# Kernel tuning notes

Measured on AMD Instinct MI355X. Metric: run time of the kernel, lower is better.

## Reference

```python
import math
import jax, jax.numpy as jnp
import numpy as np

B, S, D, H = 2, 2048, 2048, 16
HD = D // H
EPS = 1e-6


def _precompute_freqs_cis(dim, end, theta=500000.0):
    inv_freqs = 1.0 / theta ** (np.arange(0, dim, 2, dtype=np.float32) / dim)
    t = np.arange(end, dtype=np.float32)
    freqs = np.outer(t, inv_freqs).astype(np.float32)
    # [1, end, 1, dim//2, 2] matching torch stack(cos, sin, dim=4)
    return jnp.asarray(np.stack([np.cos(freqs)[None, :, None, :], np.sin(freqs)[None, :, None, :]], axis=4))


def setup_inputs() -> dict:
    key = jax.random.key(0)
    k1, k2, k3 = jax.random.split(key, 3)
    x = jax.random.normal(k1, (B, S, D), dtype=jnp.float32)
    w_qkv = jax.random.normal(k2, (3 * D, D), dtype=jnp.float32) * 0.02
    w_out = jax.random.normal(k3, (D, D), dtype=jnp.float32) * 0.02
    attn_scale = jnp.asarray(math.log2(S * S - S), dtype=jnp.float32)
    freqs_cis = _precompute_freqs_cis(HD, S)
    return {"x": x, "w_qkv": w_qkv, "w_out": w_out, "attn_scale": attn_scale, "freqs_cis": freqs_cis}


def _apply_rotary(q, k, fc):
    # q, k: [b, s, h, hd]; fc: [1, s, 1, hd//2, 2]
    b, s, h, hd = q.shape
    qk = jnp.concatenate([q, k], axis=2).reshape(b, s, 2 * h, hd // 2, 2)
    real = qk[..., 0] * fc[..., 0] - qk[..., 1] * fc[..., 1]
    imag = qk[..., 1] * fc[..., 0] + qk[..., 0] * fc[..., 1]
    rot = jnp.stack([real, imag], axis=-1).reshape(b, s, 2 * h, hd)
    return rot[:, :, :h], rot[:, :, h:]


def reference(x, w_qkv, w_out, attn_scale, freqs_cis):
    b, s, d = x.shape
    qkv = x @ w_qkv.T                      # [b, s, 3d]
    q, k, v = jnp.split(qkv, 3, axis=2)
    q = q.reshape(b, s, H, HD)
    k = k.reshape(b, s, H, HD)
    v = v.reshape(b, s, H, HD)
    q, k = _apply_rotary(q, k, freqs_cis[:, :s])
    # -> [b, h, s, hd]
    q = q.transpose(0, 2, 1, 3)
    k = k.transpose(0, 2, 1, 3)
    v = v.transpose(0, 2, 1, 3)
    # per-head L2 norm of q/k, learned scale on q
    q = q / (jnp.linalg.norm(q, axis=-1, keepdims=True) + EPS)
    k = k / (jnp.linalg.norm(k, axis=-1, keepdims=True) + EPS)
    q = q * attn_scale
    # causal SDPA with scale=1.0
    scores = jnp.einsum('bhqd,bhkd->bhqk', q, k)
    causal = jnp.tril(jnp.ones((s, s), dtype=bool))
    scores = jnp.where(causal, scores, -jnp.inf)
    attn = jax.nn.softmax(scores, axis=-1)
    out = jnp.einsum('bhqk,bhkd->bhqd', attn, v)
    out = out.transpose(0, 2, 1, 3).reshape(b, s, d)
    return out @ w_out.T
```

## Files before the change

kernel.cpp:

```cpp
#include <hip/hip_runtime.h>
#include <stdint.h>

#define B_  2
#define S_  2048
#define D_  2048
#define H_  16
#define HD_ 128
#define D3_ 6144

typedef unsigned short u16;
typedef __attribute__((ext_vector_type(8))) __bf16 bf16x8;
typedef __attribute__((ext_vector_type(4))) float f32x4;
typedef __attribute__((ext_vector_type(8))) u16  u16x8;
typedef __attribute__((ext_vector_type(2))) u16  u16x2;

__device__ inline u16 f2bf(float f) {
  union { float f; uint32_t u; } v; v.f = f;
  uint32_t r = v.u + 0x7FFFu + ((v.u >> 16) & 1u);
  return (u16)(r >> 16);
}
__device__ inline float bf2f(u16 u) {
  union { float f; uint32_t u; } v; v.u = ((uint32_t)u) << 16;
  return v.f;
}
__device__ inline void gload_lds16(const void* g, void* l) {
  __builtin_amdgcn_global_load_lds((const __attribute__((address_space(1))) uint32_t*)g,
                                   (__attribute__((address_space(3))) uint32_t*)l, 16, 0, 0);
}

#define TILE_SYNC() do { \
    asm volatile("s_waitcnt lgkmcnt(0)" ::: "memory"); \
    asm volatile("s_waitcnt vmcnt(0)" ::: "memory"); \
    __builtin_amdgcn_s_barrier(); \
    asm volatile("" ::: "memory"); \
  } while (0)

__global__ __launch_bounds__(256) void castk(const float* __restrict__ in, u16* __restrict__ out, int n) {
  int i = blockIdx.x * 256 + threadIdx.x;
  int n8 = n >> 3;
  if (i < n8) {
    f32x4 a = ((const f32x4*)in)[2*i];
    f32x4 b = ((const f32x4*)in)[2*i + 1];
    u16x8 o;
#pragma unroll
    for (int j = 0; j < 4; ++j) o[j] = f2bf(a[j]);
#pragma unroll
    for (int j = 0; j < 4; ++j) o[4+j] = f2bf(b[j]);
    ((u16x8*)out)[i] = o;
  }
}

template<int BF16OUT>
__global__ __launch_bounds__(512, 2) void gemm8(const u16* __restrict__ A, const u16* __restrict__ Bw,
                                                void* __restrict__ Cp, int M, int N, int K) {
  __shared__ __align__(16) u16 lds_[65536];
  char* ldsb = (char*)lds_;
  const int tid = threadIdx.x;
  const int w = tid >> 6, l = tid & 63;
  const int lr = l & 15, lg = l >> 4;
  const int wr = w >> 2, wc = w & 3;
  const int nbn = (int)gridDim.x;
  const int nwg = nbn * (int)gridDim.y;
  const int bid = (int)(blockIdx.y * gridDim.x + blockIdx.x);
  const int swz = (bid & 7) * (nwg >> 3) + (bid >> 3);
  const int bm = swz / nbn, bn = swz % nbn;

  f32x4 acc[8][4] = {};

  int row4[4], col4[4];
#pragma unroll
  for (int i = 0; i < 4; ++i) {
    int off = i*8192 + tid*16;
    row4[i] = off >> 7;
    col4[i] = (off & 127) ^ ((row4[i] & 7) << 4);
  }
  const size_t rs = (size_t)K * 2;
  const char* Ab = (const char*)A + (size_t)bm * 256 * rs;
  const char* Bb = (const char*)Bw + (size_t)bn * 256 * rs;
  const int wb = w * 1024;

#define STG(T_) do { \
    char* dA_ = ldsb + ((T_)&1)*32768; \
    char* dB_ = ldsb + 65536 + ((T_)&1)*32768; \
    _Pragma("unroll") \
    for (int i_ = 0; i_ < 4; ++i_) \
      gload_lds16(Ab + (size_t)row4[i_]*rs + (size_t)(T_)*128 + col4[i_], dA_ + i_*8192 + wb); \
    _Pragma("unroll") \
    for (int i_ = 0; i_ < 4; ++i_) \
      gload_lds16(Bb + (size_t)row4[i_]*rs + (size_t)(T_)*128 + col4[i_], dB_ + i_*8192 + wb); \
  } while (0)

#define RD_A(dst, mf, ks) do { int row_ = wr*128 + (mf)*16 + lr; \
    dst = *(const bf16x8*)(La + row_*128 + (((ks)*64 + lg*16) ^ ((row_ & 7) << 4))); } while (0)
#define RD_B(dst, nf, ks) do { int row_ = wc*64 + (nf)*16 + lr; \
    dst = *(const bf16x8*)(Lb + row_*128 + (((ks)*64 + lg*16) ^ ((row_ & 7) << 4))); } while (0)

  const int NT = K >> 6;
  STG(0);
  TILE_SYNC();

  for (int T = 0; T < NT; ++T) {
    const char* La = ldsb + (T & 1)*32768;
    const char* Lb = ldsb + 65536 + (T & 1)*32768;
    if (T + 1 < NT) STG(T + 1);

    bf16x8 a0[4], a1[4], b0[4], b1[4];
#pragma unroll
    for (int mf = 0; mf < 4; ++mf) { RD_A(a0[mf], mf, 0); RD_A(a1[mf], mf, 1); }
#pragma unroll
    for (int nf = 0; nf < 4; ++nf) { RD_B(b0[nf], nf, 0); RD_B(b1[nf], nf, 1); }
#pragma unroll
    for (int mf = 0; mf < 4; ++mf)
#pragma unroll
      for (int nf = 0; nf < 4; ++nf) {
        acc[mf][nf] = __builtin_amdgcn_mfma_f32_16x16x32_bf16(a0[mf], b0[nf], acc[mf][nf], 0, 0, 0);
        acc[mf][nf] = __builtin_amdgcn_mfma_f32_16x16x32_bf16(a1[mf], b1[nf], acc[mf][nf], 0, 0, 0);
      }
#pragma unroll
    for (int mf = 0; mf < 4; ++mf) { RD_A(a0[mf], mf + 4, 0); RD_A(a1[mf], mf + 4, 1); }
#pragma unroll
    for (int mf = 0; mf < 4; ++mf)
#pragma unroll
      for (int nf = 0; nf < 4; ++nf) {
        acc[mf+4][nf] = __builtin_amdgcn_mfma_f32_16x16x32_bf16(a0[mf], b0[nf], acc[mf+4][nf], 0, 0, 0);
        acc[mf+4][nf] = __builtin_amdgcn_mfma_f32_16x16x32_bf16(a1[mf], b1[nf], acc[mf+4][nf], 0, 0, 0);
      }
    TILE_SYNC();
  }
#undef STG
#undef RD_A
#undef RD_B

#pragma unroll
  for (int mf = 0; mf < 8; ++mf)
#pragma unroll
    for (int nf = 0; nf < 4; ++nf)
#pragma unroll
      for (int j = 0; j < 4; ++j) {
        int m = bm*256 + wr*128 + mf*16 + lg*4 + j;
        int n = bn*256 + wc*64 + nf*16 + lr;
        float v = acc[mf][nf][j];
        if (BF16OUT) ((u16*)Cp)[(size_t)m * N + n] = f2bf(v);
        else         ((float*)Cp)[(size_t)m * N + n] = v;
      }
}

template<int BF16OUT>
__global__ __launch_bounds__(256, 2) void gemm_bt(const u16* __restrict__ A, const u16* __restrict__ Bw,
                                                  void* __restrict__ Cp, int M, int N, int K) {
  __shared__ __align__(16) u16 lds_[32768];
  char* ldsb = (char*)lds_;
  const int tid = threadIdx.x;
  const int w = tid >> 6, l = tid & 63;
  const int lr = l & 15, lg = l >> 4;
  const int nwg = (int)(gridDim.x * gridDim.y);
  const int bid = (int)(blockIdx.y * gridDim.x + blockIdx.x);
  const int swz = (bid & 7) * (nwg >> 3) + (bid >> 3);
  const int bm = swz / (int)gridDim.x, bn = swz % (int)gridDim.x;
  const int wr = w >> 1, wc = w & 1;

  f32x4 acc[4][4] = {};

  int row4[4], col4[4];
#pragma unroll
  for (int i = 0; i < 4; ++i) {
    int off = i*4096 + tid*16;
    row4[i] = off >> 7;
    col4[i] = (off & 127) ^ ((row4[i] & 7) << 4);
  }
  const size_t rs = (size_t)K * 2;
  const char* Ab = (const char*)A + (size_t)bm * 128 * rs;
  const char* Bb = (const char*)Bw + (size_t)bn * 128 * rs;
  const int wb = w * 1024;

#define STG(T_) do { \
    char* dA_ = ldsb + ((T_)&1)*16384; \
    char* dB_ = ldsb + 32768 + ((T_)&1)*16384; \
    _Pragma("unroll") \
    for (int i_ = 0; i_ < 4; ++i_) \
      gload_lds16(Ab + (size_t)row4[i_]*rs + (size_t)(T_)*128 + col4[i_], dA_ + i_*4096 + wb); \
    _Pragma("unroll") \
    for (int i_ = 0; i_ < 4; ++i_) \
      gload_lds16(Bb + (size_t)row4[i_]*rs + (size_t)(T_)*128 + col4[i_], dB_ + i_*4096 + wb); \
  } while (0)

  const int NT = K >> 6;
  STG(0);
  TILE_SYNC();

  for (int T = 0; T < NT; ++T) {
    const char* La = ldsb + (T & 1)*16384;
    const char* Lb = ldsb + 32768 + (T & 1)*16384;
    if (T + 1 < NT) STG(T + 1);

    bf16x8 af[4][2], bf[4][2];
#pragma unroll
    for (int mt = 0; mt < 4; ++mt) {
      int row = wr*64 + mt*16 + lr;
#pragma unroll
      for (int ks = 0; ks < 2; ++ks)
        af[mt][ks] = *(const bf16x8*)(La + row*128 + ((ks*64 + lg*16) ^ ((row & 7) << 4)));
    }
#pragma unroll
    for (int nt = 0; nt < 4; ++nt) {
      int row = wc*64 + nt*16 + lr;
#pragma unroll
      for (int ks = 0; ks < 2; ++ks)
        bf[nt][ks] = *(const bf16x8*)(Lb + row*128 + ((ks*64 + lg*16) ^ ((row & 7) << 4)));
    }
#pragma unroll
    for (int mt = 0; mt < 4; ++mt)
#pragma unroll
      for (int nt = 0; nt < 4; ++nt)
#pragma unroll
        for (int ks = 0; ks < 2; ++ks)
          acc[mt][nt] = __builtin_amdgcn_mfma_f32_16x16x32_bf16(af[mt][ks], bf[nt][ks], acc[mt][nt], 0, 0, 0);
    TILE_SYNC();
  }
#undef STG

#pragma unroll
  for (int mt = 0; mt < 4; ++mt)
#pragma unroll
    for (int nt = 0; nt < 4; ++nt)
#pragma unroll
      for (int j = 0; j < 4; ++j) {
        int m = bm*128 + wr*64 + mt*16 + lg*4 + j;
        int n = bn*128 + wc*64 + nt*16 + lr;
        float v = acc[mt][nt][j];
        if (BF16OUT) ((u16*)Cp)[(size_t)m * N + n] = f2bf(v);
        else         ((float*)Cp)[(size_t)m * N + n] = v;
      }
}

__global__ __launch_bounds__(256) void rope_norm(const u16* __restrict__ qkv, const float* __restrict__ fc,
                                                 const float* __restrict__ scale_p,
                                                 u16* __restrict__ Qo, u16* __restrict__ Ko) {
  int gid = blockIdx.x;
  int bs = gid >> 2;
  int s = bs & (S_ - 1);
  int b = bs >> 11;
  int w = threadIdx.x >> 6, l = threadIdx.x & 63;
  int h = (gid & 3)*4 + w;
  float2 cs = ((const float2*)fc)[(size_t)s*64 + l];
  float scale = scale_p[0] * 1.4426950408889634f;
  const u16* base = qkv + (size_t)bs * D3_;
  size_t obase = ((size_t)(b*H_ + h) * S_ + s) * HD_ + 2*l;
  {
    const u16* p = base + h*HD_ + 2*l;
    float x0 = bf2f(p[0]), x1 = bf2f(p[1]);
    float r0 = x0*cs.x - x1*cs.y;
    float r1 = x1*cs.x + x0*cs.y;
    float t = r0*r0 + r1*r1;
#pragma unroll
    for (int mk = 1; mk < 64; mk <<= 1) t += __shfl_xor(t, mk, 64);
    float inv = scale / (sqrtf(t) + 1e-6f);
    u16x2 o; o[0] = f2bf(r0*inv); o[1] = f2bf(r1*inv);
    *(u16x2*)(Qo + obase) = o;
  }
  {
    const u16* p = base + D_ + h*HD_ + 2*l;
    float x0 = bf2f(p[0]), x1 = bf2f(p[1]);
    float r0 = x0*cs.x - x1*cs.y;
    float r1 = x1*cs.x + x0*cs.y;
    float t = r0*r0 + r1*r1;
#pragma unroll
    for (int mk = 1; mk < 64; mk <<= 1) t += __shfl_xor(t, mk, 64);
    float inv = 1.0f / (sqrtf(t) + 1e-6f);
    u16x2 o; o[0] = f2bf(r0*inv); o[1] = f2bf(r1*inv);
    *(u16x2*)(Ko + obase) = o;
  }
}

__global__ __launch_bounds__(256) void v_trans(const u16* __restrict__ qkv, u16* __restrict__ Vt) {
  __shared__ u16 vt[64][136];
  int blk = blockIdx.x;
  int bh = blk >> 5, st = blk & 31;
  int b = bh >> 4, h = bh & 15;
  int s0 = st * 64;
  int tid = threadIdx.x;
#pragma unroll
  for (int i = 0; i < 4; ++i) {
    int idx = tid + i*256;
    int row = idx >> 4, ch = idx & 15;
    u16x8 v = *(const u16x8*)(qkv + (size_t)(b*S_ + s0 + row) * D3_ + 2*D_ + h*HD_ + ch*8);
    *(u16x8*)(&vt[row][ch*8]) = v;
  }
  __syncthreads();
#pragma unroll
  for (int p = 0; p < 2; ++p) {
    int d = p*64 + (tid >> 2);
    int q = (tid & 3) * 16;
    u16x8 t0, t1;
#pragma unroll
    for (int i = 0; i < 8; ++i) t0[i] = vt[q + i][d];
#pragma unroll
    for (int i = 0; i < 8; ++i) t1[i] = vt[q + 8 + i][d];
    u16* dst = Vt + ((size_t)bh * HD_ + d) * S_ + s0 + q;
    *(u16x8*)dst = t0;
    *(u16x8*)(dst + 8) = t1;
  }
}

__global__ __launch_bounds__(512) void flash_attn(const u16* __restrict__ Qh, const u16* __restrict__ Kh,
                                                  const u16* __restrict__ Vt, u16* __restrict__ AO) {
  __shared__ __align__(16) u16 lK[2][64*128];
  __shared__ __align__(16) u16 lV[128*64];
  __shared__ __align__(16) u16 lP[8][16*72];
  const int i0 = (int)blockIdx.x;
  const int k5 = i0 & 255;
  const int bh = k5 >> 3;
  const int jj = k5 & 7;
  const int qt = (i0 < 256) ? (15 - jj) : jj;
  const int tid = threadIdx.x, w = tid >> 6, l = tid & 63;
  const int lr = l & 15, lg = l >> 4;
  const int b = bh >> 4, h = bh & 15;

  bf16x8 qf[4];
  {
    const u16* qp = Qh + ((size_t)bh * S_ + qt*128 + w*16 + lr) * HD_ + lg*8;
#pragma unroll
    for (int ks = 0; ks < 4; ++ks) qf[ks] = *(const bf16x8*)(qp + ks*32);
  }
  float m[4], ls[4];
  f32x4 oacc[8] = {};
#pragma unroll
  for (int j = 0; j < 4; ++j) { m[j] = -__builtin_inff(); ls[j] = 0.f; }

  int krow[2], kcol[2], vrow[2], vcol[2], dstb[2];
#pragma unroll
  for (int p = 0; p < 2; ++p) {
    int off = p*8192 + tid*16;
    krow[p] = off >> 8; kcol[p] = (off & 255) ^ ((krow[p] & 7) << 4);
    vrow[p] = off >> 7; vcol[p] = (off & 127) ^ ((vrow[p] & 7) << 4);
    dstb[p] = p*8192 + w*1024;
  }
  const char* Kb = (const char*)(Kh + (size_t)bh * S_ * HD_);
  const char* Vb = (const char*)(Vt + (size_t)bh * HD_ * S_);

#define STAGE_K(nb, kt_) do {                                                       \
    _Pragma("unroll")                                                               \
    for (int p_ = 0; p_ < 2; ++p_)                                                  \
      gload_lds16(Kb + (size_t)((kt_)*64 + krow[p_])*256 + kcol[p_],                \
                  (char*)lK[nb] + dstb[p_]);                                        \
  } while (0)
#define STAGE_V(kt_) do {                                                           \
    _Pragma("unroll")                                                               \
    for (int p_ = 0; p_ < 2; ++p_)                                                  \
      gload_lds16(Vb + (size_t)vrow[p_]*(S_*2) + (kt_)*128 + vcol[p_],              \
                  (char*)lV + dstb[p_]);                                            \
  } while (0)

  const int nt = 2*qt + 2;
  STAGE_K(0, 0);
  STAGE_V(0);
  int cur = 0;
  for (int kt = 0; kt < nt; ++kt) {
    asm volatile("s_waitcnt vmcnt(2)" ::: "memory");
    __builtin_amdgcn_s_barrier();
    asm volatile("" ::: "memory");
    const char* lKb = (const char*)lK[cur];

    f32x4 sc[4] = {};
    __builtin_amdgcn_s_setprio(1);
#pragma unroll
    for (int f = 0; f < 4; ++f) {
      int row = f*16 + lr;
#pragma unroll
      for (int ks = 0; ks < 4; ++ks) {
        bf16x8 kf = *(const bf16x8*)(lKb + row*256 + ((ks*64 + lg*16) ^ ((row & 7) << 4)));
        sc[f] = __builtin_amdgcn_mfma_f32_16x16x32_bf16(qf[ks], kf, sc[f], 0, 0, 0);
      }
    }
    __builtin_amdgcn_s_setprio(0);
    if (kt < nt-1) STAGE_K(cur ^ 1, kt + 1);

    if (kt >= nt-2) {
#pragma unroll
      for (int f = 0; f < 4; ++f)
#pragma unroll
        for (int j = 0; j < 4; ++j)
          if (kt*64 + f*16 + lr > qt*128 + w*16 + lg*4 + j) sc[f][j] = -__builtin_inff();
    }
    float rm[4], resc[4], rowp[4];
#pragma unroll
    for (int j = 0; j < 4; ++j) {
      rm[j] = fmaxf(fmaxf(sc[0][j], sc[1][j]), fmaxf(sc[2][j], sc[3][j]));
      rm[j] = fmaxf(rm[j], __shfl_xor(rm[j], 1, 64));
      rm[j] = fmaxf(rm[j], __shfl_xor(rm[j], 2, 64));
      rm[j] = fmaxf(rm[j], __shfl_xor(rm[j], 4, 64));
      rm[j] = fmaxf(rm[j], __shfl_xor(rm[j], 8, 64));
      float mn = fmaxf(m[j], rm[j]);
      resc[j] = exp2f(m[j] - mn);
      m[j] = mn;
      rowp[j] = 0.f;
    }
#pragma unroll
    for (int f = 0; f < 4; ++f)
#pragma unroll
      for (int j = 0; j < 4; ++j) {
        float p = exp2f(sc[f][j] - m[j]);
        sc[f][j] = p;
        rowp[j] += p;
      }
#pragma unroll
    for (int j = 0; j < 4; ++j) {
      rowp[j] += __shfl_xor(rowp[j], 1, 64);
      rowp[j] += __shfl_xor(rowp[j], 2, 64);
      rowp[j] += __shfl_xor(rowp[j], 4, 64);
      rowp[j] += __shfl_xor(rowp[j], 8, 64);
      ls[j] = ls[j] * resc[j] + rowp[j];
    }
#pragma unroll
    for (int fd = 0; fd < 8; ++fd)
#pragma unroll
      for (int j = 0; j < 4; ++j) oacc[fd][j] *= resc[j];
#pragma unroll
    for (int f = 0; f < 4; ++f)
#pragma unroll
      for (int j = 0; j < 4; ++j)
        lP[w][(lg*4 + j)*72 + f*16 + lr] = f2bf(sc[f][j]);

    if (kt < nt-1) { asm volatile("s_waitcnt vmcnt(2)" ::: "memory"); }
    else           { asm volatile("s_waitcnt vmcnt(0)" ::: "memory"); }
    __builtin_amdgcn_s_barrier();
    asm volatile("" ::: "memory");
    __builtin_amdgcn_s_setprio(1);
#pragma unroll
    for (int ks = 0; ks < 2; ++ks) {
      bf16x8 pf = *(const bf16x8*)((const char*)lP[w] + lr*144 + ks*64 + lg*16);
#pragma unroll
      for (int fd = 0; fd < 8; ++fd) {
        int row = fd*16 + lr;
        bf16x8 vf = *(const bf16x8*)((const char*)lV + row*128 + ((ks*64 + lg*16) ^ ((row & 7) << 4)));
        oacc[fd] = __builtin_amdgcn_mfma_f32_16x16x32_bf16(pf, vf, oacc[fd], 0, 0, 0);
      }
    }
    __builtin_amdgcn_s_setprio(0);
    asm volatile("" ::: "memory");
    __builtin_amdgcn_s_barrier();
    asm volatile("" ::: "memory");
    if (kt < nt-1) STAGE_V(kt + 1);
    cur ^= 1;
  }
#undef STAGE_K
#undef STAGE_V
  float invl[4];
#pragma unroll
  for (int j = 0; j < 4; ++j) invl[j] = 1.0f / ls[j];
#pragma unroll
  for (int fd = 0; fd < 8; ++fd)
#pragma unroll
    for (int j = 0; j < 4; ++j) {
      int qq = qt*128 + w*16 + lg*4 + j;
      int dd = fd*16 + lr;
      float v = oacc[fd][j] * invl[j];
      AO[((size_t)b*S_ + qq)*D_ + h*HD_ + dd] = f2bf(v);
    }
}

extern "C" void kernel_launch(void* const* d_in, const int* in_sizes, int n_in,
                              void* d_out, int out_size, void* d_ws, size_t ws_size,
                              hipStream_t stream) {
  const float* x        = (const float*)d_in[0];
  const float* w_qkv    = (const float*)d_in[1];
  const float* w_out    = (const float*)d_in[2];
  const float* attn_sc  = (const float*)d_in[3];
  const float* freqs    = (const float*)d_in[4];

  if (ws_size < 167772160u) return;

  char* ws = (char*)d_ws;
  u16* xbf  = (u16*)(ws);
  u16* wqbf = (u16*)(ws + 16777216);
  u16* wobf = (u16*)(ws + 41943040);
  u16* qkv  = (u16*)(ws + 50331648);
  u16* Qh   = (u16*)(ws + 100663296);
  u16* Kh   = (u16*)(ws + 117440512);
  u16* Vt   = (u16*)(ws + 134217728);
  u16* AO   = (u16*)(ws + 150994944);

  castk<<<4096, 256, 0, stream>>>(x,     xbf,  8388608);
  castk<<<6144, 256, 0, stream>>>(w_qkv, wqbf, 12582912);
  castk<<<2048, 256, 0, stream>>>(w_out, wobf, 4194304);

  gemm8<1><<<dim3(24, 16), 512, 0, stream>>>(xbf, wqbf, qkv, 4096, 6144, 2048);

  rope_norm<<<16384, 256, 0, stream>>>(qkv, freqs, attn_sc, Qh, Kh);
  v_trans<<<1024, 256, 0, stream>>>(qkv, Vt);

  flash_attn<<<512, 512, 0, stream>>>(Qh, Kh, Vt, AO);

  gemm_bt<0><<<dim3(16, 32), 256, 0, stream>>>(AO, wobf, (float*)d_out, 4096, 2048, 2048);
}
```

Before: 297.9 us.

## Shrink QKV GEMM tile to 256x128 and interleave MFMA accumulator chains

The QKV projection GEMM goes from a 256x256 block tile to 256x128. Waves are rearranged 4x2, each covering 64x64, and the launch grid doubles to 768 blocks to reduce wave-quantization imbalance across CUs. The MFMA issue order in gemm8, gemm_bt and the flash-attention QK loop is reordered so consecutive MFMAs target different accumulators, avoiding back-to-back dependency stalls. The cost is more global and LDS traffic per FLOP from the smaller N tile.

```diff
diff --git a/kernel.cpp b/kernel.cpp
--- a/kernel.cpp
+++ b/kernel.cpp
@@ -53,47 +53,48 @@
 template<int BF16OUT>
 __global__ __launch_bounds__(512, 2) void gemm8(const u16* __restrict__ A, const u16* __restrict__ Bw,
                                                 void* __restrict__ Cp, int M, int N, int K) {
-  __shared__ __align__(16) u16 lds_[65536];
+  __shared__ __align__(16) u16 lds_[49152];
   char* ldsb = (char*)lds_;
   const int tid = threadIdx.x;
   const int w = tid >> 6, l = tid & 63;
   const int lr = l & 15, lg = l >> 4;
-  const int wr = w >> 2, wc = w & 3;
+  const int wr = w >> 1, wc = w & 1;
   const int nbn = (int)gridDim.x;
   const int nwg = nbn * (int)gridDim.y;
   const int bid = (int)(blockIdx.y * gridDim.x + blockIdx.x);
   const int swz = (bid & 7) * (nwg >> 3) + (bid >> 3);
   const int bm = swz / nbn, bn = swz % nbn;
 
-  f32x4 acc[8][4] = {};
-
-  int row4[4], col4[4];
+  f32x4 acc[4][4] = {};
+
+  int rowA[4], colA[4], rowB[2], colB[2];
 #pragma unroll
   for (int i = 0; i < 4; ++i) {
     int off = i*8192 + tid*16;
-    row4[i] = off >> 7;
-    col4[i] = (off & 127) ^ ((row4[i] & 7) << 4);
+    rowA[i] = off >> 7;
+    colA[i] = (off & 127) ^ ((rowA[i] & 7) << 4);
+  }
+#pragma unroll
+  for (int i = 0; i < 2; ++i) {
+    int off = i*8192 + tid*16;
+    rowB[i] = off >> 7;
+    colB[i] = (off & 127) ^ ((rowB[i] & 7) << 4);
   }
   const size_t rs = (size_t)K * 2;
   const char* Ab = (const char*)A + (size_t)bm * 256 * rs;
-  const char* Bb = (const char*)Bw + (size_t)bn * 256 * rs;
+  const char* Bb = (const char*)Bw + (size_t)bn * 128 * rs;
   const int wb = w * 1024;
 
 #define STG(T_) do { \
     char* dA_ = ldsb + ((T_)&1)*32768; \
-    char* dB_ = ldsb + 65536 + ((T_)&1)*32768; \
+    char* dB_ = ldsb + 65536 + ((T_)&1)*16384; \
     _Pragma("unroll") \
     for (int i_ = 0; i_ < 4; ++i_) \
-      gload_lds16(Ab + (size_t)row4[i_]*rs + (size_t)(T_)*128 + col4[i_], dA_ + i_*8192 + wb); \
+      gload_lds16(Ab + (size_t)rowA[i_]*rs + (size_t)(T_)*128 + colA[i_], dA_ + i_*8192 + wb); \
     _Pragma("unroll") \
-    for (int i_ = 0; i_ < 4; ++i_) \
-      gload_lds16(Bb + (size_t)row4[i_]*rs + (size_t)(T_)*128 + col4[i_], dB_ + i_*8192 + wb); \
+    for (int i_ = 0; i_ < 2; ++i_) \
+      gload_lds16(Bb + (size_t)rowB[i_]*rs + (size_t)(T_)*128 + colB[i_], dB_ + i_*8192 + wb); \
   } while (0)
-
-#define RD_A(dst, mf, ks) do { int row_ = wr*128 + (mf)*16 + lr; \
-    dst = *(const bf16x8*)(La + row_*128 + (((ks)*64 + lg*16) ^ ((row_ & 7) << 4))); } while (0)
-#define RD_B(dst, nf, ks) do { int row_ = wc*64 + (nf)*16 + lr; \
-    dst = *(const bf16x8*)(Lb + row_*128 + (((ks)*64 + lg*16) ^ ((row_ & 7) << 4))); } while (0)
 
   const int NT = K >> 6;
   STG(0);
@@ -101,44 +102,44 @@
 
   for (int T = 0; T < NT; ++T) {
     const char* La = ldsb + (T & 1)*32768;
-    const char* Lb = ldsb + 65536 + (T & 1)*32768;
+    const char* Lb = ldsb + 65536 + (T & 1)*16384;
     if (T + 1 < NT) STG(T + 1);
 
     bf16x8 a0[4], a1[4], b0[4], b1[4];
 #pragma unroll
-    for (int mf = 0; mf < 4; ++mf) { RD_A(a0[mf], mf, 0); RD_A(a1[mf], mf, 1); }
-#pragma unroll
-    for (int nf = 0; nf < 4; ++nf) { RD_B(b0[nf], nf, 0); RD_B(b1[nf], nf, 1); }
+    for (int mf = 0; mf < 4; ++mf) {
+      int row = wr*64 + mf*16 + lr;
+      a0[mf] = *(const bf16x8*)(La + row*128 + ((lg*16)      ^ ((row & 7) << 4)));
+      a1[mf] = *(const bf16x8*)(La + row*128 + ((64 + lg*16) ^ ((row & 7) << 4)));
+    }
+#pragma unroll
+    for (int nf = 0; nf < 4; ++nf) {
+      int row = wc*64 + nf*16 + lr;
+      b0[nf] = *(const bf16x8*)(Lb + row*128 + ((lg*16)      ^ ((row & 7) << 4)));
+      b1[nf] = *(const bf16x8*)(Lb + row*128 + ((64 + lg*16) ^ ((row & 7) << 4)));
+    }
 #pragma unroll
     for (int mf = 0; mf < 4; ++mf)
 #pragma unroll
-      for (int nf = 0; nf < 4; ++nf) {
+      for (int nf = 0; nf < 4; ++nf)
         acc[mf][nf] = __builtin_amdgcn_mfma_f32_16x16x32_bf16(a0[mf], b0[nf], acc[mf][nf], 0, 0, 0);
+#pragma unroll
+    for (int mf = 0; mf < 4; ++mf)
+#pragma unroll
+      for (int nf = 0; nf < 4; ++nf)
         acc[mf][nf] = __builtin_amdgcn_mfma_f32_16x16x32_bf16(a1[mf], b1[nf], acc[mf][nf], 0, 0, 0);
-      }
-#pragma unroll
-    for (int mf = 0; mf < 4; ++mf) { RD_A(a0[mf], mf + 4, 0); RD_A(a1[mf], mf + 4, 1); }
-#pragma unroll
-    for (int mf = 0; mf < 4; ++mf)
-#pragma unroll
-      for (int nf = 0; nf < 4; ++nf) {
-        acc[mf+4][nf] = __builtin_amdgcn_mfma_f32_16x16x32_bf16(a0[mf], b0[nf], acc[mf+4][nf], 0, 0, 0);
-        acc[mf+4][nf] = __builtin_amdgcn_mfma_f32_16x16x32_bf16(a1[mf], b1[nf], acc[mf+4][nf], 0, 0, 0);
-      }
     TILE_SYNC();
   }
 #undef STG
-#undef RD_A
-#undef RD_B
-
-#pragma unroll
-  for (int mf = 0; mf < 8; ++mf)
+
+#pragma unroll
+  for (int mf = 0; mf < 4; ++mf)
 #pragma unroll
     for (int nf = 0; nf < 4; ++nf)
 #pragma unroll
       for (int j = 0; j < 4; ++j) {
-        int m = bm*256 + wr*128 + mf*16 + lg*4 + j;
-        int n = bn*256 + wc*64 + nf*16 + lr;
+        int m = bm*256 + wr*64 + mf*16 + lg*4 + j;
+        int n = bn*128 + wc*64 + nf*16 + lr;
         float v = acc[mf][nf][j];
         if (BF16OUT) ((u16*)Cp)[(size_t)m * N + n] = f2bf(v);
         else         ((float*)Cp)[(size_t)m * N + n] = v;
@@ -212,9 +213,12 @@
     for (int mt = 0; mt < 4; ++mt)
 #pragma unroll
       for (int nt = 0; nt < 4; ++nt)
-#pragma unroll
-        for (int ks = 0; ks < 2; ++ks)
-          acc[mt][nt] = __builtin_amdgcn_mfma_f32_16x16x32_bf16(af[mt][ks], bf[nt][ks], acc[mt][nt], 0, 0, 0);
+        acc[mt][nt] = __builtin_amdgcn_mfma_f32_16x16x32_bf16(af[mt][0], bf[nt][0], acc[mt][nt], 0, 0, 0);
+#pragma unroll
+    for (int mt = 0; mt < 4; ++mt)
+#pragma unroll
+      for (int nt = 0; nt < 4; ++nt)
+        acc[mt][nt] = __builtin_amdgcn_mfma_f32_16x16x32_bf16(af[mt][1], bf[nt][1], acc[mt][nt], 0, 0, 0);
     TILE_SYNC();
   }
 #undef STG
@@ -364,10 +368,10 @@
     f32x4 sc[4] = {};
     __builtin_amdgcn_s_setprio(1);
 #pragma unroll
-    for (int f = 0; f < 4; ++f) {
-      int row = f*16 + lr;
-#pragma unroll
-      for (int ks = 0; ks < 4; ++ks) {
+    for (int ks = 0; ks < 4; ++ks) {
+#pragma unroll
+      for (int f = 0; f < 4; ++f) {
+        int row = f*16 + lr;
         bf16x8 kf = *(const bf16x8*)(lKb + row*256 + ((ks*64 + lg*16) ^ ((row & 7) << 4)));
         sc[f] = __builtin_amdgcn_mfma_f32_16x16x32_bf16(qf[ks], kf, sc[f], 0, 0, 0);
       }
@@ -484,7 +488,7 @@
   castk<<<6144, 256, 0, stream>>>(w_qkv, wqbf, 12582912);
   castk<<<2048, 256, 0, stream>>>(w_out, wobf, 4194304);
 
-  gemm8<1><<<dim3(24, 16), 512, 0, stream>>>(xbf, wqbf, qkv, 4096, 6144, 2048);
+  gemm8<1><<<dim3(48, 16), 512, 0, stream>>>(xbf, wqbf, qkv, 4096, 6144, 2048);
 
   rope_norm<<<16384, 256, 0, stream>>>(qkv, freqs, attn_sc, Qh, Kh);
   v_trans<<<1024, 256, 0, stream>>>(qkv, Vt);
```

After: 293.9 us. No clear change (-1.4%).

## Transpose QK^T MFMA so softmax rows are lane-local; reorder GEMM MFMA issue

Applied to the files above, without the earlier changes.

In attention, the QK^T MFMA operands are swapped so each lane holds one query row's scores across its accumulator registers. Row max and sum then need only two cross-lane shuffles instead of four per row element. The rescale factors are broadcast back with shuffles, and P is written to LDS with 8-byte packed stores. Both GEMM kernels also load all A fragments up front and issue the MFMAs in two k-step passes to lengthen dependency distance, at the cost of more live registers.

```diff
diff --git a/kernel.cpp b/kernel.cpp
--- a/kernel.cpp
+++ b/kernel.cpp
@@ -12,6 +12,7 @@
 typedef __attribute__((ext_vector_type(8))) __bf16 bf16x8;
 typedef __attribute__((ext_vector_type(4))) float f32x4;
 typedef __attribute__((ext_vector_type(8))) u16  u16x8;
+typedef __attribute__((ext_vector_type(4))) u16  u16x4;
 typedef __attribute__((ext_vector_type(2))) u16  u16x2;
 
 __device__ inline u16 f2bf(float f) {
@@ -104,27 +105,21 @@
     const char* Lb = ldsb + 65536 + (T & 1)*32768;
     if (T + 1 < NT) STG(T + 1);
 
-    bf16x8 a0[4], a1[4], b0[4], b1[4];
-#pragma unroll
-    for (int mf = 0; mf < 4; ++mf) { RD_A(a0[mf], mf, 0); RD_A(a1[mf], mf, 1); }
+    bf16x8 a0[8], a1[8], b0[4], b1[4];
+#pragma unroll
+    for (int mf = 0; mf < 8; ++mf) { RD_A(a0[mf], mf, 0); RD_A(a1[mf], mf, 1); }
 #pragma unroll
     for (int nf = 0; nf < 4; ++nf) { RD_B(b0[nf], nf, 0); RD_B(b1[nf], nf, 1); }
 #pragma unroll
-    for (int mf = 0; mf < 4; ++mf)
-#pragma unroll
-      for (int nf = 0; nf < 4; ++nf) {
+    for (int mf = 0; mf < 8; ++mf)
+#pragma unroll
+      for (int nf = 0; nf < 4; ++nf)
         acc[mf][nf] = __builtin_amdgcn_mfma_f32_16x16x32_bf16(a0[mf], b0[nf], acc[mf][nf], 0, 0, 0);
+#pragma unroll
+    for (int mf = 0; mf < 8; ++mf)
+#pragma unroll
+      for (int nf = 0; nf < 4; ++nf)
         acc[mf][nf] = __builtin_amdgcn_mfma_f32_16x16x32_bf16(a1[mf], b1[nf], acc[mf][nf], 0, 0, 0);
-      }
-#pragma unroll
-    for (int mf = 0; mf < 4; ++mf) { RD_A(a0[mf], mf + 4, 0); RD_A(a1[mf], mf + 4, 1); }
-#pragma unroll
-    for (int mf = 0; mf < 4; ++mf)
-#pragma unroll
-      for (int nf = 0; nf < 4; ++nf) {
-        acc[mf+4][nf] = __builtin_amdgcn_mfma_f32_16x16x32_bf16(a0[mf], b0[nf], acc[mf+4][nf], 0, 0, 0);
-        acc[mf+4][nf] = __builtin_amdgcn_mfma_f32_16x16x32_bf16(a1[mf], b1[nf], acc[mf+4][nf], 0, 0, 0);
-      }
     TILE_SYNC();
   }
 #undef STG
@@ -212,9 +207,12 @@
     for (int mt = 0; mt < 4; ++mt)
 #pragma unroll
       for (int nt = 0; nt < 4; ++nt)
-#pragma unroll
-        for (int ks = 0; ks < 2; ++ks)
-          acc[mt][nt] = __builtin_amdgcn_mfma_f32_16x16x32_bf16(af[mt][ks], bf[nt][ks], acc[mt][nt], 0, 0, 0);
+        acc[mt][nt] = __builtin_amdgcn_mfma_f32_16x16x32_bf16(af[mt][0], bf[nt][0], acc[mt][nt], 0, 0, 0);
+#pragma unroll
+    for (int mt = 0; mt < 4; ++mt)
+#pragma unroll
+      for (int nt = 0; nt < 4; ++nt)
+        acc[mt][nt] = __builtin_amdgcn_mfma_f32_16x16x32_bf16(af[mt][1], bf[nt][1], acc[mt][nt], 0, 0, 0);
     TILE_SYNC();
   }
 #undef STG
@@ -322,10 +320,8 @@
 #pragma unroll
     for (int ks = 0; ks < 4; ++ks) qf[ks] = *(const bf16x8*)(qp + ks*32);
   }
-  float m[4], ls[4];
+  float m0 = -__builtin_inff(), ls0 = 0.f;
   f32x4 oacc[8] = {};
-#pragma unroll
-  for (int j = 0; j < 4; ++j) { m[j] = -__builtin_inff(); ls[j] = 0.f; }
 
   int krow[2], kcol[2], vrow[2], vcol[2], dstb[2];
 #pragma unroll
@@ -364,12 +360,12 @@
     f32x4 sc[4] = {};
     __builtin_amdgcn_s_setprio(1);
 #pragma unroll
-    for (int f = 0; f < 4; ++f) {
-      int row = f*16 + lr;
-#pragma unroll
-      for (int ks = 0; ks < 4; ++ks) {
+    for (int ks = 0; ks < 4; ++ks) {
+#pragma unroll
+      for (int f = 0; f < 4; ++f) {
+        int row = f*16 + lr;
         bf16x8 kf = *(const bf16x8*)(lKb + row*256 + ((ks*64 + lg*16) ^ ((row & 7) << 4)));
-        sc[f] = __builtin_amdgcn_mfma_f32_16x16x32_bf16(qf[ks], kf, sc[f], 0, 0, 0);
+        sc[f] = __builtin_amdgcn_mfma_f32_16x16x32_bf16(kf, qf[ks], sc[f], 0, 0, 0);
       }
     }
     __builtin_amdgcn_s_setprio(0);
@@ -380,46 +376,44 @@
       for (int f = 0; f < 4; ++f)
 #pragma unroll
         for (int j = 0; j < 4; ++j)
-          if (kt*64 + f*16 + lr > qt*128 + w*16 + lg*4 + j) sc[f][j] = -__builtin_inff();
-    }
-    float rm[4], resc[4], rowp[4];
-#pragma unroll
-    for (int j = 0; j < 4; ++j) {
-      rm[j] = fmaxf(fmaxf(sc[0][j], sc[1][j]), fmaxf(sc[2][j], sc[3][j]));
-      rm[j] = fmaxf(rm[j], __shfl_xor(rm[j], 1, 64));
-      rm[j] = fmaxf(rm[j], __shfl_xor(rm[j], 2, 64));
-      rm[j] = fmaxf(rm[j], __shfl_xor(rm[j], 4, 64));
-      rm[j] = fmaxf(rm[j], __shfl_xor(rm[j], 8, 64));
-      float mn = fmaxf(m[j], rm[j]);
-      resc[j] = exp2f(m[j] - mn);
-      m[j] = mn;
-      rowp[j] = 0.f;
-    }
+          if (kt*64 + f*16 + lg*4 + j > qt*128 + w*16 + lr) sc[f][j] = -__builtin_inff();
+    }
+    float pmax = sc[0][0];
 #pragma unroll
     for (int f = 0; f < 4; ++f)
 #pragma unroll
+      for (int j = 0; j < 4; ++j) pmax = fmaxf(pmax, sc[f][j]);
+    pmax = fmaxf(pmax, __shfl_xor(pmax, 16, 64));
+    pmax = fmaxf(pmax, __shfl_xor(pmax, 32, 64));
+    float mn = fmaxf(m0, pmax);
+    float resc = exp2f(m0 - mn);
+    m0 = mn;
+    float rsum = 0.f;
+#pragma unroll
+    for (int f = 0; f < 4; ++f)
+#pragma unroll
       for (int j = 0; j < 4; ++j) {
-        float p = exp2f(sc[f][j] - m[j]);
+        float p = exp2f(sc[f][j] - mn);
         sc[f][j] = p;
-        rowp[j] += p;
+        rsum += p;
       }
-#pragma unroll
-    for (int j = 0; j < 4; ++j) {
-      rowp[j] += __shfl_xor(rowp[j], 1, 64);
-      rowp[j] += __shfl_xor(rowp[j], 2, 64);
-      rowp[j] += __shfl_xor(rowp[j], 4, 64);
-      rowp[j] += __shfl_xor(rowp[j], 8, 64);
-      ls[j] = ls[j] * resc[j] + rowp[j];
-    }
+    rsum += __shfl_xor(rsum, 16, 64);
+    rsum += __shfl_xor(rsum, 32, 64);
+    ls0 = ls0 * resc + rsum;
+    float rescj[4];
+#pragma unroll
+    for (int j = 0; j < 4; ++j) rescj[j] = __shfl(resc, lg*4 + j, 64);
 #pragma unroll
     for (int fd = 0; fd < 8; ++fd)
 #pragma unroll
-      for (int j = 0; j < 4; ++j) oacc[fd][j] *= resc[j];
-#pragma unroll
-    for (int f = 0; f < 4; ++f)
-#pragma unroll
-      for (int j = 0; j < 4; ++j)
-        lP[w][(lg*4 + j)*72 + f*16 + lr] = f2bf(sc[f][j]);
+      for (int j = 0; j < 4; ++j) oacc[fd][j] *= rescj[j];
+#pragma unroll
+    for (int f = 0; f < 4; ++f) {
+      u16x4 pk;
+#pragma unroll
+      for (int j = 0; j < 4; ++j) pk[j] = f2bf(sc[f][j]);
+      *(u16x4*)((char*)lP[w] + lr*144 + f*32 + lg*8) = pk;
+    }
 
     if (kt < nt-1) { asm volatile("s_waitcnt vmcnt(2)" ::: "memory"); }
     else           { asm volatile("s_waitcnt vmcnt(0)" ::: "memory"); }
@@ -447,7 +441,10 @@
 #undef STAGE_V
   float invl[4];
 #pragma unroll
-  for (int j = 0; j < 4; ++j) invl[j] = 1.0f / ls[j];
+  for (int j = 0; j < 4; ++j) {
+    float lsj = __shfl(ls0, lg*4 + j, 64);
+    invl[j] = 1.0f / lsj;
+  }
 #pragma unroll
   for (int fd = 0; fd < 8; ++fd)
 #pragma unroll
```

After: 278.1 us. 1.07x faster.
